# Kernel tuning notes

Hardware: AMD Instinct MI355X
Metric: run time of the kernel (lower is better)

## Reference

```python
import jax, jax.numpy as jnp
import numpy as np

K = 1024      # num_embeddings
D = 256       # embedding_dim
BETA = 0.25


def setup_inputs() -> dict:
    key = jax.random.key(0)
    k1, k2 = jax.random.split(key)
    latents = jax.random.normal(k1, (32, D, 32, 32), dtype=jnp.float32)
    # nn.Embedding weight init: uniform(-1/K, 1/K)
    weight = jax.random.uniform(k2, (K, D), dtype=jnp.float32,
                                minval=-1.0 / K, maxval=1.0 / K)
    return {"latents": latents, "weight": weight}


def reference(latents, weight):
    # NCHW -> NHWC
    lat = jnp.transpose(latents, (0, 2, 3, 1))          # [B,H,W,D]
    lat_shape = lat.shape
    flat = lat.reshape(-1, D)                           # [N,D]

    dist = (jnp.sum(flat ** 2, axis=1, keepdims=True)
            - 2.0 * jnp.matmul(flat, weight.T)
            + jnp.sum(weight ** 2, axis=1))             # [N,K]

    min_ind = jnp.argmin(dist, axis=1)                  # [N]
    min_embed = jax.nn.one_hot(min_ind, K, dtype=flat.dtype)  # [N,K]

    # one-hot @ weight == direct gather
    z_q = jnp.take(weight, min_ind, axis=0).reshape(lat_shape)  # [B,H,W,D]

    sg = jax.lax.stop_gradient
    loss = (jnp.mean((sg(z_q) - lat) ** 2)
            + BETA * jnp.mean((z_q - sg(lat)) ** 2))

    # straight-through estimator
    z_q_st = lat + sg(z_q - lat)

    e_mean = jnp.mean(min_embed, axis=0)                # [K]
    perplexity = jnp.exp(-jnp.sum(e_mean * jnp.log(e_mean + 1e-10)))

    z_q_out = jnp.transpose(z_q_st, (0, 3, 1, 2))       # NHWC -> NCHW
    return (loss, z_q_out, perplexity, min_embed, min_ind[:, None])
```

## Files before the change

kernel.cpp:

```cpp
#include <hip/hip_runtime.h>

#define KN 1024
#define DD 256
#define NTOT 32768
#define HW 1024

#define OFF_LOSS 0
#define OFF_ZQ   1
#define OFF_PERP 8388609
#define OFF_EMB  8388610
#define OFF_IND  41943042

#define WS_WSUM2_OFF 4112
#define WS_WBH_OFF   8208
#define WS_WBL_OFF   (8208 + 524288)

#define XS_STRIDE 260
#define THR 3.0e-4f

typedef __bf16 bf16x8 __attribute__((ext_vector_type(8)));
typedef float  f32x4  __attribute__((ext_vector_type(4)));
typedef float  f32x2  __attribute__((ext_vector_type(2)));
typedef unsigned short ushort_t;

#define SM_XS    0
#define SM_XFH   33280
#define SM_XFL   49664
#define SM_WSC   66048
#define SM_PART  70144
#define SM_REDV  70144
#define SM_ROWM  72192
#define SM_CCNT  72320
#define SM_CLIST 72448
#define SM_FV    73472
#define SM_ASUM  74496
#define SM_BI    74624
#define SM_LRED  74752
#define SM_SIZE  74784

__device__ __forceinline__ unsigned short bf16_rne(float f) {
    unsigned u = __float_as_uint(f);
    return (unsigned short)((u + 0x7FFFu + ((u >> 16) & 1u)) >> 16);
}

__device__ __forceinline__ float exact_dist(const float* xs, const float* wsC,
                                            const float* asum,
                                            const float* __restrict__ w,
                                            int r, int k) {
    float a = 0.f;
    const float4* wr = (const float4*)(w + k * DD);
    const float4* xr = (const float4*)(xs + r * XS_STRIDE);
    #pragma unroll 4
    for (int q = 0; q < 64; ++q) {
        const float4 wv = wr[q];
        const float4 xv = xr[q];
        a = fmaf(xv.x, wv.x, a);
        a = fmaf(xv.y, wv.y, a);
        a = fmaf(xv.z, wv.z, a);
        a = fmaf(xv.w, wv.w, a);
    }
    return (asum[r] - 2.0f * a) + wsC[k];
}

__global__ __launch_bounds__(256) void vq_prep(const float* __restrict__ w,
                                               float* __restrict__ wsum2,
                                               ushort_t* __restrict__ wBh,
                                               ushort_t* __restrict__ wBl) {
    const int k = blockIdx.x;
    const int d = threadIdx.x;
    float v = w[k * DD + d];
    {
        const int c = k >> 4, s0 = d >> 5, g = (d >> 3) & 3, j = d & 7;
        const int lane = (k & 15) | (g << 4);
        const int idx = (((c * 8 + s0) * 64 + lane) << 3) + j;
        const unsigned short hh = bf16_rne(v);
        wBh[idx] = hh;
        wBl[idx] = bf16_rne(v - __uint_as_float((unsigned)hh << 16));
    }
    float s = v * v;
    #pragma unroll
    for (int off = 32; off; off >>= 1) s += __shfl_down(s, off, 64);
    __shared__ float wsum[4];
    const int wave = d >> 6, lane = d & 63;
    if (lane == 0) wsum[wave] = s;
    __syncthreads();
    if (d == 0) wsum2[k] = (wsum[0] + wsum[1]) + (wsum[2] + wsum[3]);
}

__global__ __launch_bounds__(1024) void vq_main(const float* __restrict__ lat,
                                                const float* __restrict__ w,
                                                const float* __restrict__ wsum2,
                                                const ushort_t* __restrict__ wBh,
                                                const ushort_t* __restrict__ wBl,
                                                float* __restrict__ out,
                                                unsigned* __restrict__ cnt,
                                                double* __restrict__ lossSum) {
    extern __shared__ char smem[];
    float*    xs    = (float*)(smem + SM_XS);
    ushort_t* xfH   = (ushort_t*)(smem + SM_XFH);
    ushort_t* xfL   = (ushort_t*)(smem + SM_XFL);
    float*    wsC   = (float*)(smem + SM_WSC);
    float*    part  = (float*)(smem + SM_PART);
    float*    redv  = (float*)(smem + SM_REDV);
    float*    rowm  = (float*)(smem + SM_ROWM);
    unsigned* ccnt  = (unsigned*)(smem + SM_CCNT);
    int*      clist = (int*)(smem + SM_CLIST);
    float*    fv    = (float*)(smem + SM_FV);
    float*    asum  = (float*)(smem + SM_ASUM);
    int*      bi    = (int*)(smem + SM_BI);
    double*   lred  = (double*)(smem + SM_LRED);

    const int n0  = blockIdx.x * 32;
    const int b   = n0 >> 10;
    const int hw0 = n0 & 1023;
    const int tid = threadIdx.x;
    const int l   = tid & 63;
    const int wv  = tid >> 6;

    {
        const float* base = lat + (size_t)b * (DD * HW) + hw0;
        const int rr = tid & 31, dl = tid >> 5;
        #pragma unroll
        for (int it = 0; it < 8; ++it) {
            const int d = it * 32 + dl;
            xs[rr * XS_STRIDE + d] = __builtin_nontemporal_load(&base[d * HW + rr]);
        }
        if (tid < KN) wsC[tid] = wsum2[tid];
    }
    __syncthreads();

    #pragma unroll
    for (int h = 0; h < 2; ++h) {
        if (tid < 256) {
            const int r = tid & 15, seg = tid >> 4;
            float p = 0.f;
            #pragma unroll
            for (int i = 0; i < 16; ++i) {
                float x = xs[(h * 16 + r) * XS_STRIDE + seg * 16 + i];
                p += x * x;
            }
            part[seg * 17 + r] = p;
        }
        __syncthreads();
        if (tid < 16) {
            float a = 0.f;
            #pragma unroll
            for (int s = 0; s < 16; ++s) a += part[s * 17 + tid];
            asum[h * 16 + tid] = a;
        }
        __syncthreads();
    }

    {
        const int u  = tid;
        const int rt = u >> 9, s0 = (u >> 6) & 7, ll = u & 63;
        const int row = rt * 16 + (ll & 15);
        const int d0  = s0 * 32 + (ll >> 4) * 8;
        const float4 x0 = *(const float4*)(xs + row * XS_STRIDE + d0);
        const float4 x1 = *(const float4*)(xs + row * XS_STRIDE + d0 + 4);
        float xv[8] = {x0.x, x0.y, x0.z, x0.w, x1.x, x1.y, x1.z, x1.w};
        unsigned hh[8], lo[8];
        #pragma unroll
        for (int j = 0; j < 8; ++j) {
            hh[j] = bf16_rne(xv[j]);
            lo[j] = bf16_rne(xv[j] - __uint_as_float(hh[j] << 16));
        }
        uint4 ph, pl;
        ph.x = hh[0] | (hh[1] << 16); ph.y = hh[2] | (hh[3] << 16);
        ph.z = hh[4] | (hh[5] << 16); ph.w = hh[6] | (hh[7] << 16);
        pl.x = lo[0] | (lo[1] << 16); pl.y = lo[2] | (lo[3] << 16);
        pl.z = lo[4] | (lo[5] << 16); pl.w = lo[6] | (lo[7] << 16);
        *(uint4*)(xfH + u * 8) = ph;
        *(uint4*)(xfL + u * 8) = pl;
    }
    __syncthreads();

    f32x4 acc[2][4];
    #pragma unroll
    for (int rt = 0; rt < 2; ++rt)
        #pragma unroll
        for (int c = 0; c < 4; ++c)
            acc[rt][c] = (f32x4){0.f, 0.f, 0.f, 0.f};

    {
        bf16x8 ah0, ah1, al0, al1;
        bf16x8 pbh0, pbl0, pbh1, pbl1;

        #define BOFF(s0_, c_) (((size_t)(((wv * 4 + (c_)) * 8 + (s0_)) * 64 + l)) * 8)
        pbh0 = *(const bf16x8*)(wBh + BOFF(0, 0));
        pbl0 = *(const bf16x8*)(wBl + BOFF(0, 0));
        pbh1 = *(const bf16x8*)(wBh + BOFF(0, 1));
        pbl1 = *(const bf16x8*)(wBl + BOFF(0, 1));

        #pragma unroll
        for (int it = 0; it < 32; ++it) {
            const int s0 = it >> 2, c = it & 3;
            if (c == 0) {
                ah0 = *(const bf16x8*)(xfH + ((0 * 8 + s0) * 64 + l) * 8);
                ah1 = *(const bf16x8*)(xfH + ((1 * 8 + s0) * 64 + l) * 8);
                al0 = *(const bf16x8*)(xfL + ((0 * 8 + s0) * 64 + l) * 8);
                al1 = *(const bf16x8*)(xfL + ((1 * 8 + s0) * 64 + l) * 8);
            }
            bf16x8 bh, bl;
            if ((it & 1) == 0) { bh = pbh0; bl = pbl0; } else { bh = pbh1; bl = pbl1; }
            if (it + 2 < 32) {
                const int nit = it + 2, ns = nit >> 2, nc = nit & 3;
                if ((it & 1) == 0) {
                    pbh0 = *(const bf16x8*)(wBh + BOFF(ns, nc));
                    pbl0 = *(const bf16x8*)(wBl + BOFF(ns, nc));
                } else {
                    pbh1 = *(const bf16x8*)(wBh + BOFF(ns, nc));
                    pbl1 = *(const bf16x8*)(wBl + BOFF(ns, nc));
                }
            }
            acc[0][c] = __builtin_amdgcn_mfma_f32_16x16x32_bf16(ah0, bh, acc[0][c], 0, 0, 0);
            acc[1][c] = __builtin_amdgcn_mfma_f32_16x16x32_bf16(ah1, bh, acc[1][c], 0, 0, 0);
            acc[0][c] = __builtin_amdgcn_mfma_f32_16x16x32_bf16(ah0, bl, acc[0][c], 0, 0, 0);
            acc[1][c] = __builtin_amdgcn_mfma_f32_16x16x32_bf16(ah1, bl, acc[1][c], 0, 0, 0);
            acc[0][c] = __builtin_amdgcn_mfma_f32_16x16x32_bf16(al0, bh, acc[0][c], 0, 0, 0);
            acc[1][c] = __builtin_amdgcn_mfma_f32_16x16x32_bf16(al1, bh, acc[1][c], 0, 0, 0);
        }
        #undef BOFF
    }

    float rmv[2][4];
    #pragma unroll
    for (int rt = 0; rt < 2; ++rt)
        #pragma unroll
        for (int q = 0; q < 4; ++q) rmv[rt][q] = 3.4e38f;
    #pragma unroll
    for (int c = 0; c < 4; ++c) {
        const float cv = wsC[(wv * 4 + c) * 16 + (l & 15)];
        #pragma unroll
        for (int rt = 0; rt < 2; ++rt) {
            #pragma unroll
            for (int q = 0; q < 4; ++q) {
                const float dv = fmaf(-2.0f, acc[rt][c][q], cv);
                acc[rt][c][q] = dv;
                rmv[rt][q] = fminf(rmv[rt][q], dv);
            }
        }
    }
    #pragma unroll
    for (int rt = 0; rt < 2; ++rt)
        #pragma unroll
        for (int q = 0; q < 4; ++q) {
            float m = rmv[rt][q];
            #pragma unroll
            for (int off = 1; off < 16; off <<= 1) m = fminf(m, __shfl_xor(m, off, 64));
            rmv[rt][q] = m;
        }
    if ((l & 15) == 0) {
        const int g = l >> 4;
        #pragma unroll
        for (int rt = 0; rt < 2; ++rt)
            #pragma unroll
            for (int q = 0; q < 4; ++q)
                redv[wv * 32 + rt * 16 + g * 4 + q] = rmv[rt][q];
    }
    __syncthreads();
    if (tid < 32) {
        float m = redv[tid];
        #pragma unroll
        for (int ww = 1; ww < 16; ++ww) m = fminf(m, redv[ww * 32 + tid]);
        rowm[tid] = m;
        ccnt[tid] = 0u;
    }
    __syncthreads();

    #pragma unroll
    for (int rt = 0; rt < 2; ++rt) {
        #pragma unroll
        for (int q = 0; q < 4; ++q) {
            const int row = rt * 16 + ((l >> 4) << 2) + q;
            const float lim = rowm[row] + THR;
            #pragma unroll
            for (int c = 0; c < 4; ++c) {
                if (acc[rt][c][q] <= lim) {
                    const unsigned pos = atomicAdd(&ccnt[row], 1u);
                    if (pos < 8) clist[row * 8 + pos] = (wv * 4 + c) * 16 + (l & 15);
                }
            }
        }
    }
    __syncthreads();

    if (tid < 256) {
        const int r = tid >> 3, ci = tid & 7;
        const unsigned cc = ccnt[r];
        if (cc >= 2u) {
            if (cc <= 8u) {
                if ((unsigned)ci < cc)
                    fv[r * 8 + ci] = exact_dist(xs, wsC, asum, w, r, clist[r * 8 + ci]);
            } else if (ci == 0) {
                float bvv = 3.4e38f; int bkk = 0;
                for (int k = 0; k < KN; ++k) {
                    const float dvv = exact_dist(xs, wsC, asum, w, r, k);
                    if (dvv < bvv) { bvv = dvv; bkk = k; }
                }
                bi[r] = bkk;
            }
        }
    }
    __syncthreads();
    if (tid < 32) {
        const unsigned cc = ccnt[tid];
        int kk;
        if (cc == 1u) kk = clist[tid * 8];
        else if (cc <= 8u) {
            float v = fv[tid * 8]; kk = clist[tid * 8];
            for (unsigned ci = 1; ci < cc; ++ci) {
                const float ov = fv[tid * 8 + ci];
                const int   ok = clist[tid * 8 + ci];
                if (ov < v || (ov == v && ok < kk)) { v = ov; kk = ok; }
            }
        } else kk = bi[tid];
        bi[tid] = kk;
        __builtin_nontemporal_store((float)kk, &out[OFF_IND + n0 + tid]);
        atomicAdd(&cnt[kk], 1u);
    }
    __syncthreads();

    {
        f32x2* emb2 = reinterpret_cast<f32x2*>(out + OFF_EMB) + (size_t)n0 * (KN / 2);
        #pragma unroll
        for (int it = 0; it < 16; ++it) {
            const int f = it * 1024 + tid;
            const int r = f >> 9;
            const int kq = (f & 511) * 2;
            const int tt = bi[r];
            f32x2 v2;
            v2.x = (kq     == tt) ? 1.0f : 0.0f;
            v2.y = (kq + 1 == tt) ? 1.0f : 0.0f;
            __builtin_nontemporal_store(v2, &emb2[f]);
        }
    }

    #pragma unroll
    for (int h = 0; h < 2; ++h) {
        if (tid < 256) {
            const int n0h = n0 + h * 16;
            const int bb = n0h >> 10, hw0h = n0h & 1023;
            float* zq_out = out + OFF_ZQ + (size_t)bb * (DD * HW) + hw0h;
            const int jj = tid & 15, db = tid >> 4;
            const int krow = bi[h * 16 + jj];
            float lsum = 0.f;
            #pragma unroll
            for (int it = 0; it < 16; ++it) {
                const int d = it * 16 + db;
                const float latv = xs[(h * 16 + jj) * XS_STRIDE + d];
                const float zq   = w[krow * DD + d];
                const float dif  = zq - latv;
                __builtin_nontemporal_store(latv + dif, &zq_out[d * HW + jj]);
                lsum = fmaf(dif, dif, lsum);
            }
            float s2 = lsum;
            #pragma unroll
            for (int off = 32; off; off >>= 1) s2 += __shfl_down(s2, off, 64);
            if ((tid & 63) == 0) lred[wv] = (double)s2;
        }
        __syncthreads();
        if (tid == 0) {
            double t = (lred[0] + lred[1]) + (lred[2] + lred[3]);
            atomicAdd(lossSum, t);
        }
        __syncthreads();
    }
}

__global__ __launch_bounds__(1024) void vq_finalize(const unsigned* __restrict__ cnt,
                                                    const double* __restrict__ lossSum,
                                                    float* __restrict__ out) {
    const int t = threadIdx.x;
    __shared__ float red[16];
    const float e = (float)cnt[t] * (1.0f / 32768.0f);
    float s = e * logf(e + 1e-10f);
    #pragma unroll
    for (int off = 32; off; off >>= 1) s += __shfl_down(s, off, 64);
    const int wave = t >> 6, lane = t & 63;
    if (lane == 0) red[wave] = s;
    __syncthreads();
    if (t == 0) {
        float tot = 0.f;
        #pragma unroll
        for (int i = 0; i < 16; ++i) tot += red[i];
        out[OFF_PERP] = expf(-tot);
        const float m = (float)(lossSum[0] * (1.0 / 8388608.0));
        out[OFF_LOSS] = m + 0.25f * m;
    }
}

extern "C" void kernel_launch(void* const* d_in, const int* in_sizes, int n_in,
                              void* d_out, int out_size, void* d_ws, size_t ws_size,
                              hipStream_t stream) {
    const float* lat = (const float*)d_in[0];
    const float* w   = (const float*)d_in[1];

    char* ws = (char*)d_ws;
    double*   lossSum = (double*)ws;
    unsigned* cnt     = (unsigned*)(ws + 8);
    float*    wsum2   = (float*)(ws + WS_WSUM2_OFF);
    ushort_t* wBh     = (ushort_t*)(ws + WS_WBH_OFF);
    ushort_t* wBl     = (ushort_t*)(ws + WS_WBL_OFF);
    float*    out     = (float*)d_out;

    hipMemsetAsync(d_ws, 0, 4104, stream);

    hipFuncSetAttribute(reinterpret_cast<const void*>(vq_main),
                        hipFuncAttributeMaxDynamicSharedMemorySize, SM_SIZE);

    vq_prep<<<KN, 256, 0, stream>>>(w, wsum2, wBh, wBl);
    vq_main<<<NTOT / 32, 1024, SM_SIZE, stream>>>(lat, w, wsum2, wBh, wBl, out, cnt, lossSum);
    vq_finalize<<<1, 1024, 0, stream>>>(cnt, lossSum, out);
}
```

Before: 138.0 us.

## Process 64 rows per block to reuse codebook MFMA fragments across four row tiles

```diff
diff --git a/kernel.cpp b/kernel.cpp
--- a/kernel.cpp
+++ b/kernel.cpp
@@ -24,19 +24,19 @@
 typedef unsigned short ushort_t;
 
 #define SM_XS    0
-#define SM_XFH   33280
-#define SM_XFL   49664
-#define SM_WSC   66048
-#define SM_PART  70144
-#define SM_REDV  70144
-#define SM_ROWM  72192
-#define SM_CCNT  72320
-#define SM_CLIST 72448
-#define SM_FV    73472
-#define SM_ASUM  74496
-#define SM_BI    74624
-#define SM_LRED  74752
-#define SM_SIZE  74784
+#define SM_XFH   66560
+#define SM_XFL   99328
+#define SM_WSC   132096
+#define SM_PART  136192
+#define SM_REDV  136192
+#define SM_ROWM  140288
+#define SM_CCNT  140544
+#define SM_CLIST 140800
+#define SM_FV    142848
+#define SM_ASUM  144896
+#define SM_BI    145152
+#define SM_LRED  145408
+#define SM_SIZE  145440
 
 __device__ __forceinline__ unsigned short bf16_rne(float f) {
     unsigned u = __float_as_uint(f);
@@ -110,7 +110,7 @@
     int*      bi    = (int*)(smem + SM_BI);
     double*   lred  = (double*)(smem + SM_LRED);
 
-    const int n0  = blockIdx.x * 32;
+    const int n0  = blockIdx.x * 64;
     const int b   = n0 >> 10;
     const int hw0 = n0 & 1023;
     const int tid = threadIdx.x;
@@ -119,18 +119,18 @@
 
     {
         const float* base = lat + (size_t)b * (DD * HW) + hw0;
-        const int rr = tid & 31, dl = tid >> 5;
-        #pragma unroll
-        for (int it = 0; it < 8; ++it) {
-            const int d = it * 32 + dl;
+        const int rr = tid & 63, dl = tid >> 6;
+        #pragma unroll
+        for (int it = 0; it < 16; ++it) {
+            const int d = it * 16 + dl;
             xs[rr * XS_STRIDE + d] = __builtin_nontemporal_load(&base[d * HW + rr]);
         }
-        if (tid < KN) wsC[tid] = wsum2[tid];
-    }
-    __syncthreads();
-
-    #pragma unroll
-    for (int h = 0; h < 2; ++h) {
+        wsC[tid] = wsum2[tid];
+    }
+    __syncthreads();
+
+    #pragma unroll
+    for (int h = 0; h < 4; ++h) {
         if (tid < 256) {
             const int r = tid & 15, seg = tid >> 4;
             float p = 0.f;
@@ -151,8 +151,9 @@
         __syncthreads();
     }
 
-    {
-        const int u  = tid;
+    #pragma unroll
+    for (int i = 0; i < 2; ++i) {
+        const int u  = tid + i * 1024;
         const int rt = u >> 9, s0 = (u >> 6) & 7, ll = u & 63;
         const int row = rt * 16 + (ll & 15);
         const int d0  = s0 * 32 + (ll >> 4) * 8;
@@ -175,64 +176,60 @@
     }
     __syncthreads();
 
-    f32x4 acc[2][4];
-    #pragma unroll
-    for (int rt = 0; rt < 2; ++rt)
+    f32x4 acc[4][4];
+    #pragma unroll
+    for (int rt = 0; rt < 4; ++rt)
         #pragma unroll
         for (int c = 0; c < 4; ++c)
             acc[rt][c] = (f32x4){0.f, 0.f, 0.f, 0.f};
 
     {
-        bf16x8 ah0, ah1, al0, al1;
-        bf16x8 pbh0, pbl0, pbh1, pbl1;
+        bf16x8 ah[4], al[4];
+        bf16x8 cbh, cbl;
 
         #define BOFF(s0_, c_) (((size_t)(((wv * 4 + (c_)) * 8 + (s0_)) * 64 + l)) * 8)
-        pbh0 = *(const bf16x8*)(wBh + BOFF(0, 0));
-        pbl0 = *(const bf16x8*)(wBl + BOFF(0, 0));
-        pbh1 = *(const bf16x8*)(wBh + BOFF(0, 1));
-        pbl1 = *(const bf16x8*)(wBl + BOFF(0, 1));
+        cbh = *(const bf16x8*)(wBh + BOFF(0, 0));
+        cbl = *(const bf16x8*)(wBl + BOFF(0, 0));
 
         #pragma unroll
         for (int it = 0; it < 32; ++it) {
             const int s0 = it >> 2, c = it & 3;
             if (c == 0) {
-                ah0 = *(const bf16x8*)(xfH + ((0 * 8 + s0) * 64 + l) * 8);
-                ah1 = *(const bf16x8*)(xfH + ((1 * 8 + s0) * 64 + l) * 8);
-                al0 = *(const bf16x8*)(xfL + ((0 * 8 + s0) * 64 + l) * 8);
-                al1 = *(const bf16x8*)(xfL + ((1 * 8 + s0) * 64 + l) * 8);
-            }
-            bf16x8 bh, bl;
-            if ((it & 1) == 0) { bh = pbh0; bl = pbl0; } else { bh = pbh1; bl = pbl1; }
-            if (it + 2 < 32) {
-                const int nit = it + 2, ns = nit >> 2, nc = nit & 3;
-                if ((it & 1) == 0) {
-                    pbh0 = *(const bf16x8*)(wBh + BOFF(ns, nc));
-                    pbl0 = *(const bf16x8*)(wBl + BOFF(ns, nc));
-                } else {
-                    pbh1 = *(const bf16x8*)(wBh + BOFF(ns, nc));
-                    pbl1 = *(const bf16x8*)(wBl + BOFF(ns, nc));
+                #pragma unroll
+                for (int rt = 0; rt < 4; ++rt) {
+                    ah[rt] = *(const bf16x8*)(xfH + ((rt * 8 + s0) * 64 + l) * 8);
+                    al[rt] = *(const bf16x8*)(xfL + ((rt * 8 + s0) * 64 + l) * 8);
                 }
             }
-            acc[0][c] = __builtin_amdgcn_mfma_f32_16x16x32_bf16(ah0, bh, acc[0][c], 0, 0, 0);
-            acc[1][c] = __builtin_amdgcn_mfma_f32_16x16x32_bf16(ah1, bh, acc[1][c], 0, 0, 0);
-            acc[0][c] = __builtin_amdgcn_mfma_f32_16x16x32_bf16(ah0, bl, acc[0][c], 0, 0, 0);
-            acc[1][c] = __builtin_amdgcn_mfma_f32_16x16x32_bf16(ah1, bl, acc[1][c], 0, 0, 0);
-            acc[0][c] = __builtin_amdgcn_mfma_f32_16x16x32_bf16(al0, bh, acc[0][c], 0, 0, 0);
-            acc[1][c] = __builtin_amdgcn_mfma_f32_16x16x32_bf16(al1, bh, acc[1][c], 0, 0, 0);
+            const bf16x8 bh = cbh, bl = cbl;
+            if (it + 1 < 32) {
+                const int ns = (it + 1) >> 2, nc = (it + 1) & 3;
+                cbh = *(const bf16x8*)(wBh + BOFF(ns, nc));
+                cbl = *(const bf16x8*)(wBl + BOFF(ns, nc));
+            }
+            #pragma unroll
+            for (int rt = 0; rt < 4; ++rt)
+                acc[rt][c] = __builtin_amdgcn_mfma_f32_16x16x32_bf16(ah[rt], bh, acc[rt][c], 0, 0, 0);
+            #pragma unroll
+            for (int rt = 0; rt < 4; ++rt)
+                acc[rt][c] = __builtin_amdgcn_mfma_f32_16x16x32_bf16(ah[rt], bl, acc[rt][c], 0, 0, 0);
+            #pragma unroll
+            for (int rt = 0; rt < 4; ++rt)
+                acc[rt][c] = __builtin_amdgcn_mfma_f32_16x16x32_bf16(al[rt], bh, acc[rt][c], 0, 0, 0);
         }
         #undef BOFF
     }
 
-    float rmv[2][4];
-    #pragma unroll
-    for (int rt = 0; rt < 2; ++rt)
+    float rmv[4][4];
+    #pragma unroll
+    for (int rt = 0; rt < 4; ++rt)
         #pragma unroll
         for (int q = 0; q < 4; ++q) rmv[rt][q] = 3.4e38f;
     #pragma unroll
     for (int c = 0; c < 4; ++c) {
         const float cv = wsC[(wv * 4 + c) * 16 + (l & 15)];
         #pragma unroll
-        for (int rt = 0; rt < 2; ++rt) {
+        for (int rt = 0; rt < 4; ++rt) {
             #pragma unroll
             for (int q = 0; q < 4; ++q) {
                 const float dv = fmaf(-2.0f, acc[rt][c][q], cv);
@@ -242,7 +239,7 @@
         }
     }
     #pragma unroll
-    for (int rt = 0; rt < 2; ++rt)
+    for (int rt = 0; rt < 4; ++rt)
         #pragma unroll
         for (int q = 0; q < 4; ++q) {
             float m = rmv[rt][q];
@@ -253,23 +250,23 @@
     if ((l & 15) == 0) {
         const int g = l >> 4;
         #pragma unroll
-        for (int rt = 0; rt < 2; ++rt)
+        for (int rt = 0; rt < 4; ++rt)
             #pragma unroll
             for (int q = 0; q < 4; ++q)
-                redv[wv * 32 + rt * 16 + g * 4 + q] = rmv[rt][q];
-    }
-    __syncthreads();
-    if (tid < 32) {
+                redv[wv * 64 + rt * 16 + g * 4 + q] = rmv[rt][q];
+    }
+    __syncthreads();
+    if (tid < 64) {
         float m = redv[tid];
         #pragma unroll
-        for (int ww = 1; ww < 16; ++ww) m = fminf(m, redv[ww * 32 + tid]);
+        for (int ww = 1; ww < 16; ++ww) m = fminf(m, redv[ww * 64 + tid]);
         rowm[tid] = m;
         ccnt[tid] = 0u;
     }
     __syncthreads();
 
     #pragma unroll
-    for (int rt = 0; rt < 2; ++rt) {
+    for (int rt = 0; rt < 4; ++rt) {
         #pragma unroll
         for (int q = 0; q < 4; ++q) {
             const int row = rt * 16 + ((l >> 4) << 2) + q;
@@ -285,7 +282,7 @@
     }
     __syncthreads();
 
-    if (tid < 256) {
+    if (tid < 512) {
         const int r = tid >> 3, ci = tid & 7;
         const unsigned cc = ccnt[r];
         if (cc >= 2u) {
@@ -303,7 +300,7 @@
         }
     }
     __syncthreads();
-    if (tid < 32) {
+    if (tid < 64) {
         const unsigned cc = ccnt[tid];
         int kk;
         if (cc == 1u) kk = clist[tid * 8];
@@ -324,7 +321,7 @@
     {
         f32x2* emb2 = reinterpret_cast<f32x2*>(out + OFF_EMB) + (size_t)n0 * (KN / 2);
         #pragma unroll
-        for (int it = 0; it < 16; ++it) {
+        for (int it = 0; it < 32; ++it) {
             const int f = it * 1024 + tid;
             const int r = f >> 9;
             const int kq = (f & 511) * 2;
@@ -337,7 +334,7 @@
     }
 
     #pragma unroll
-    for (int h = 0; h < 2; ++h) {
+    for (int h = 0; h < 4; ++h) {
         if (tid < 256) {
             const int n0h = n0 + h * 16;
             const int bb = n0h >> 10, hw0h = n0h & 1023;
@@ -410,6 +407,6 @@
                         hipFuncAttributeMaxDynamicSharedMemorySize, SM_SIZE);
 
     vq_prep<<<KN, 256, 0, stream>>>(w, wsum2, wBh, wBl);
-    vq_main<<<NTOT / 32, 1024, SM_SIZE, stream>>>(lat, w, wsum2, wBh, wBl, out, cnt, lossSum);
+    vq_main<<<NTOT / 64, 1024, SM_SIZE, stream>>>(lat, w, wsum2, wBh, wBl, out, cnt, lossSum);
     vq_finalize<<<1, 1024, 0, stream>>>(cnt, lossSum, out);
 }
```

Result: slower. 143.2 us (+3.8%).
